# Kernel tuning notes

Hardware: AMD Instinct MI355X
Metric: run time of the kernel (lower is better)

The kernel has to match this reference:

```python
import jax, jax.numpy as jnp
import numpy as np

BETA = 1.0

def setup_inputs() -> dict:
    key = jax.random.key(0)
    k1, k2, k3 = jax.random.split(key, 3)
    B, T, G, D, V = 4, 2048, 8, 128, 1024
    inputs = jax.random.normal(k1, (B, T, G * D), dtype=jnp.float32)
    paddings = jax.random.randint(k2, (B, T), 0, 2, dtype=jnp.int32)
    codebook = jax.random.normal(k3, (V, G, D), dtype=jnp.float32)  # (V, G, D)
    return {"inputs": inputs, "paddings": paddings, "codebook": codebook}

def reference(inputs, paddings, codebook):
    B, T, _ = inputs.shape
    V, G, D = codebook.shape
    sg = jax.lax.stop_gradient
    x = inputs.reshape(B, T, G, D)
    x2 = jnp.sum(x * x, axis=-1)                      # (B,T,G)
    c2 = jnp.sum(codebook * codebook, axis=-1)        # (V,G)
    xc = jnp.einsum('btgd,vgd->btvg', x, codebook)    # (B,T,V,G) GEMM
    dist = x2[:, :, None, :] - 2.0 * xc + c2[None, None]
    ids = jnp.argmin(dist, axis=2)                    # (B,T,G) int
    # gather codebook[ids[b,t,g], g] -> (B,T,G,D)
    quantized = codebook[ids, jnp.arange(G)[None, None, :]]
    mask = (1 - paddings).astype(jnp.float32)[:, :, None, None]  # (B,T,1,1)
    msum = mask.sum()
    kmeans_loss = jnp.sum(((quantized - sg(x)) ** 2) * mask) / msum
    commitment_loss = jnp.sum(((x - sg(quantized)) ** 2) * mask) / msum
    total_loss = kmeans_loss + BETA * commitment_loss
    quantized_st = ((x + sg(quantized - x)) * mask).reshape(B, T, G * D)
    ids = jnp.where((paddings == 1)[:, :, None], -1, ids.astype(jnp.int32))
    return (ids, quantized_st, kmeans_loss, commitment_loss, total_loss)
```

## Files before the change

### kernel.cpp

```cpp
#include <hip/hip_runtime.h>
#include <math.h>

typedef _Float16 f16;
typedef f16 half8 __attribute__((ext_vector_type(8)));
typedef float f32x4 __attribute__((ext_vector_type(4)));

#define BT 8192
#define NG 8
#define ND 128
#define NV 1024
#define MARGIN  0.08f
#define MARGIN3 0.16f
#define BM 64
#define BN 64
#define NT 16
#define FULLBIT 0x40000000u

#define OUT_IDS 0
#define OUT_Q   65536
#define OUT_L   (65536 + 8388608)

#define OFF_C2A    0
#define OFF_C2B    8192
#define OFF_LOSSG  81920
#define OFF_CNT    147456
#define OFF_FLAGS  147464
#define OFF_CBH    213000
#define OFF_PART   (OFF_CBH + 524288)
#define OFF_CAND2  (OFF_PART + 64)
#define OFF_TOKMAP (OFF_CAND2 + 65536)

__device__ __forceinline__ void gll16(const f16* g, f16* l) {
    __builtin_amdgcn_global_load_lds(
        (const __attribute__((address_space(1))) unsigned int*)g,
        (__attribute__((address_space(3))) unsigned int*)l, 16, 0, 0);
}

__global__ __launch_bounds__(256) void prep_kernel(
    const float* __restrict__ cb, const int* __restrict__ pad,
    f16* __restrict__ cbh, float* __restrict__ c2a, float* __restrict__ c2b,
    int* __restrict__ ncnt, int* __restrict__ tokmap) {
    __shared__ float prod[16][16][9];
    __shared__ float rbuf[16][8];
    const int tid = threadIdx.x;
    const int rloc = tid >> 4, t = tid & 15;
    const int idx = blockIdx.x * 16 + rloc;
    const int v = idx >> 3, g = idx & 7;
    const int rl = v & 63;
    const float4* row4 = (const float4*)(cb + (size_t)idx * ND);

    if (tid < 16) {
        int tok = blockIdx.x * 16 + tid;
        if (!pad[tok]) {
            int p = atomicAdd(ncnt, 1);
            tokmap[p] = tok;
        }
    }

    float4 a = row4[t * 2], b = row4[t * 2 + 1];
    float vv[8] = {a.x, a.y, a.z, a.w, b.x, b.y, b.z, b.w};
    half8 h;
#pragma unroll
    for (int e = 0; e < 8; ++e) {
        prod[rloc][t][e] = __fmul_rn(vv[e], vv[e]);
        h[e] = (f16)vv[e];
    }
    int cn = v >> 6;
    size_t base = ((size_t)(g * 16 + cn)) * 8192 + rl * 128;
    *(half8*)(cbh + base + ((t ^ (rl & 7)) * 8)) = h;
    __syncthreads();

    if (t < 8) {
        float r = 0.f;
#pragma unroll
        for (int tt = 0; tt < 16; ++tt)
            r = __fadd_rn(r, prod[rloc][tt][t]);
        rbuf[rloc][t] = r;
    }
    __syncthreads();
    if (t == 0) {
        float s = __fadd_rn(
            __fadd_rn(__fadd_rn(rbuf[rloc][0], rbuf[rloc][1]),
                      __fadd_rn(rbuf[rloc][2], rbuf[rloc][3])),
            __fadd_rn(__fadd_rn(rbuf[rloc][4], rbuf[rloc][5]),
                      __fadd_rn(rbuf[rloc][6], rbuf[rloc][7])));
        c2a[idx] = s;
        c2b[g * NV + v] = s;
    }
}

__global__ __launch_bounds__(256) void padfill(
    const int* __restrict__ pad, float* __restrict__ out_ids,
    float* __restrict__ out_q, float* __restrict__ lossg) {
    const int tok = blockIdx.x;
    if (!pad[tok]) return;
    const int tid = threadIdx.x;
    ((float4*)(out_q + (size_t)tok * (NG * ND)))[tid] =
        make_float4(0.f, 0.f, 0.f, 0.f);
    if (tid < NG) {
        out_ids[tok * NG + tid] = -1.0f;
        lossg[tok * NG + tid] = 0.0f;
    }
}

__global__ __launch_bounds__(256, 4) void mfma_gemm(
    const float* __restrict__ x, const f16* __restrict__ cbh,
    const float* __restrict__ cb, const float* __restrict__ c2b,
    const int* __restrict__ ncnt, const int* __restrict__ tokmap,
    float* __restrict__ out_ids, float* __restrict__ out_q,
    float* __restrict__ lossg, int* __restrict__ cnt,
    int* __restrict__ flags, int* __restrict__ cand2) {
    __shared__ __align__(16) f16 Bh[2][BN * ND];
    __shared__ __align__(16) float c2s[NV];
    __shared__ int idsL[BM];
    __shared__ int tokL[BM];

    const int tid = threadIdx.x;
    const int b = blockIdx.x;
    const int g = b & 7;
    const int count = *ncnt;
    const int tile_base = (b >> 3) * BM;
    if (tile_base >= count) return;
    const int lane = tid & 63;
    const int w = tid >> 6;
    const int wr = w & 1, wc = w >> 1;
    const int l15 = lane & 15, l4 = lane >> 4;

    ((float4*)c2s)[tid] = ((const float4*)(c2b + (size_t)g * NV))[tid];
    {
        const f16* sh = cbh + ((size_t)(g * 16 + 0)) * 8192;
#pragma unroll
        for (int it = 0; it < 4; ++it)
            gll16(sh + it * 2048 + tid * 8, &Bh[0][it * 2048 + tid * 8]);
    }

    int tokA_[2];
#pragma unroll
    for (int ti = 0; ti < 2; ++ti) {
        int slot = tile_base + wr * 32 + ti * 16 + l15;
        tokA_[ti] = tokmap[(slot < count) ? slot : 0];
    }

    half8 ah[4][2];
#pragma unroll
    for (int kk = 0; kk < 4; ++kk)
#pragma unroll
        for (int ti = 0; ti < 2; ++ti) {
            const float* ap = x + ((size_t)tokA_[ti] * NG + g) * ND
                              + kk * 32 + l4 * 8;
            float4 p0 = *(const float4*)ap, p1 = *(const float4*)(ap + 4);
            float vv[8] = {p0.x, p0.y, p0.z, p0.w, p1.x, p1.y, p1.z, p1.w};
            half8 h;
#pragma unroll
            for (int j = 0; j < 8; ++j) h[j] = (f16)vv[j];
            ah[kk][ti] = h;
        }

    float d1s[2][4], d2s[2][4], d3s[2][4];
    int id1s[2][4], id2s[2][4];
#pragma unroll
    for (int ti = 0; ti < 2; ++ti)
#pragma unroll
        for (int r = 0; r < 4; ++r) {
            d1s[ti][r] = INFINITY;
            d2s[ti][r] = INFINITY;
            d3s[ti][r] = INFINITY;
            id1s[ti][r] = 0;
            id2s[ti][r] = 0;
        }

    int buf = 0;
#pragma unroll 1
    for (int t = 0; t < NT; ++t) {
        asm volatile("s_waitcnt vmcnt(0) lgkmcnt(0)" ::: "memory");
        __builtin_amdgcn_s_barrier();
        __builtin_amdgcn_sched_barrier(0);

        if (t + 1 < NT) {
            const f16* sh = cbh + ((size_t)(g * 16 + t + 1)) * 8192;
#pragma unroll
            for (int it = 0; it < 4; ++it)
                gll16(sh + it * 2048 + tid * 8,
                      &Bh[buf ^ 1][it * 2048 + tid * 8]);
        }

        f32x4 acc[2][2];
#pragma unroll
        for (int ti = 0; ti < 2; ++ti)
#pragma unroll
            for (int tj = 0; tj < 2; ++tj)
                acc[ti][tj] = (f32x4){0.f, 0.f, 0.f, 0.f};

#pragma unroll
        for (int kk = 0; kk < 4; ++kk) {
            half8 bh[2];
#pragma unroll
            for (int tj = 0; tj < 2; ++tj) {
                int rw = wc * 32 + tj * 16 + l15;
                bh[tj] = *(const half8*)(
                    &Bh[buf][rw * 128 + (((kk * 4 + l4) ^ (rw & 7)) << 3)]);
            }
#pragma unroll
            for (int ti = 0; ti < 2; ++ti)
#pragma unroll
                for (int tj = 0; tj < 2; ++tj)
                    acc[ti][tj] = __builtin_amdgcn_mfma_f32_16x16x32_f16(
                        ah[kk][ti], bh[tj], acc[ti][tj], 0, 0, 0);
        }

#pragma unroll
        for (int tj = 0; tj < 2; ++tj) {
            int code = t * BN + wc * 32 + tj * 16 + l15;
            float c2v = c2s[code];
#pragma unroll
            for (int ti = 0; ti < 2; ++ti)
#pragma unroll
                for (int r = 0; r < 4; ++r) {
                    float dv = fmaf(-2.0f, acc[ti][tj][r], c2v);
                    bool lt1 = dv < d1s[ti][r];
                    bool lt2 = dv < d2s[ti][r];
                    bool lt3 = dv < d3s[ti][r];
                    d3s[ti][r] = lt2 ? d2s[ti][r] : (lt3 ? dv : d3s[ti][r]);
                    d2s[ti][r] = lt1 ? d1s[ti][r] : (lt2 ? dv : d2s[ti][r]);
                    id2s[ti][r] = lt1 ? id1s[ti][r] : (lt2 ? code : id2s[ti][r]);
                    d1s[ti][r] = lt1 ? dv : d1s[ti][r];
                    id1s[ti][r] = lt1 ? code : id1s[ti][r];
                }
        }
        buf ^= 1;
    }

    __syncthreads();
    float4* red = (float4*)&Bh[0][0];
    float* redd3 = (float*)(red + 128);
#pragma unroll
    for (int ti = 0; ti < 2; ++ti)
#pragma unroll
        for (int r = 0; r < 4; ++r) {
            float d1 = d1s[ti][r], d2 = d2s[ti][r], d3 = d3s[ti][r];
            int i1 = id1s[ti][r], i2 = id2s[ti][r];
#pragma unroll
            for (int m = 1; m < 16; m <<= 1) {
                float od1 = __shfl_xor(d1, m);
                float od2 = __shfl_xor(d2, m);
                float od3 = __shfl_xor(d3, m);
                int oi1 = __shfl_xor(i1, m);
                int oi2 = __shfl_xor(i2, m);
                bool ow = od1 < d1;
                float w1 = ow ? od1 : d1, w2 = ow ? od2 : d2, w3 = ow ? od3 : d3;
                int wi1 = ow ? oi1 : i1, wi2 = ow ? oi2 : i2;
                float l1 = ow ? d1 : od1, l2 = ow ? d2 : od2;
                int li1 = ow ? i1 : oi1;
                d1 = w1; i1 = wi1;
                bool t2 = w2 < l1;
                d2 = t2 ? w2 : l1;
                i2 = t2 ? wi2 : li1;
                d3 = t2 ? fminf(w3, l1) : fminf(w2, l2);
            }
            if (l15 == 0) {
                int o = wc * BM + wr * 32 + ti * 16 + l4 * 4 + r;
                red[o] = make_float4(d1, __int_as_float(i1), d2,
                                     __int_as_float(i2));
                redd3[o] = d3;
            }
        }
    __syncthreads();

    if (tid < BM) {
        float4 A = red[tid], C = red[BM + tid];
        float a3 = redd3[tid], c3 = redd3[BM + tid];
        float a1 = A.x, a2 = A.z, c1 = C.x, c2q = C.z;
        int ai1 = __float_as_int(A.y), ai2 = __float_as_int(A.w);
        int ci1 = __float_as_int(C.y), ci2 = __float_as_int(C.w);
        bool cw = c1 < a1;
        float w1 = cw ? c1 : a1, w2 = cw ? c2q : a2, w3 = cw ? c3 : a3;
        int wi1 = cw ? ci1 : ai1, wi2 = cw ? ci2 : ai2;
        float l1 = cw ? a1 : c1, l2 = cw ? a2 : c2q;
        int li1 = cw ? ai1 : ci1;
        float d1 = w1;
        int i1 = wi1;
        bool t2 = w2 < l1;
        float d2 = t2 ? w2 : l1;
        int i2 = t2 ? wi2 : li1;
        float d3 = t2 ? fminf(w3, l1) : fminf(w2, l2);

        int slot = tile_base + tid;
        if (slot < count) {
            int tok = tokmap[slot];
            int idx = tok * NG + g;
            out_ids[idx] = (float)i1;
            idsL[tid] = i1;
            tokL[tid] = tok;
            if (d2 - d1 < MARGIN) {
                int pos = atomicAdd(cnt, 1);
                flags[pos] = idx;
                cand2[idx] = i2 | ((d3 - d1 < MARGIN3) ? (int)FULLBIT : 0);
            }
        } else {
            idsL[tid] = -1;
        }
    }
    __syncthreads();

#pragma unroll
    for (int it = 0; it < 8; ++it) {
        int i = it * 256 + tid;
        int tl = i >> 5, d4 = i & 31;
        int id = idsL[tl];
        if (id >= 0) {
            int tok = tokL[tl];
            size_t rowo = ((size_t)tok * NG + g) * ND;
            float4 q = ((const float4*)(cb + ((size_t)id * NG + g) * ND))[d4];
            float4 a = ((const float4*)(x + rowo))[d4];
            float e0 = q.x - a.x, e1 = q.y - a.y;
            float e2 = q.z - a.z, e3 = q.w - a.w;
            float s = e0 * e0 + e1 * e1 + e2 * e2 + e3 * e3;
            ((float4*)(out_q + rowo))[d4] = q;
#pragma unroll
            for (int m = 1; m < 32; m <<= 1) s += __shfl_xor(s, m);
            if (d4 == 0) lossg[tok * NG + g] = s;
        }
    }
}

__global__ __launch_bounds__(256) void recheck(
    const float* __restrict__ x, const float* __restrict__ cb,
    const float* __restrict__ c2w, const int* __restrict__ cnt,
    const int* __restrict__ flags, const int* __restrict__ cand2,
    float* __restrict__ out_ids, float* __restrict__ out_q,
    float* __restrict__ lossg) {
    __shared__ __align__(16) float xs[ND];
    __shared__ float2 redw[4];
    __shared__ int bidS;
    const int tid = threadIdx.x;
    const int lane = tid & 63;
    const int w = tid >> 6;
    const int n_f = cnt[0];

    for (int f = blockIdx.x * 4 + w; f < n_f; f += gridDim.x * 4) {
        int idx = flags[f];
        unsigned cc = (unsigned)cand2[idx];
        if (cc & FULLBIT) continue;
        int g = idx & 7;
        int id1 = (int)out_ids[idx];
        int id2 = (int)(cc & ~FULLBIT);
        float2 xv = ((const float2*)(x + (size_t)idx * ND))[lane];
        float2 av = ((const float2*)(cb + ((size_t)id1 * NG + g) * ND))[lane];
        float2 bv = ((const float2*)(cb + ((size_t)id2 * NG + g) * ND))[lane];
        float eA0 = xv.x - av.x, eA1 = xv.y - av.y;
        float eB0 = xv.x - bv.x, eB1 = xv.y - bv.y;
        float sA = eA0 * eA0 + eA1 * eA1;
        float sB = eB0 * eB0 + eB1 * eB1;
#pragma unroll
        for (int m = 1; m < 64; m <<= 1) {
            sA += __shfl_xor(sA, m);
            sB += __shfl_xor(sB, m);
        }
        int win;
        float sw;
        if (sA < sB) { win = id1; sw = sA; }
        else if (sB < sA) { win = id2; sw = sB; }
        else { win = (id1 < id2) ? id1 : id2; sw = sA; }
        if (win != id1) {
            if (lane == 0) {
                out_ids[idx] = (float)win;
                lossg[idx] = sw;
            }
            if (lane < 32) {
                float4 q = ((const float4*)(cb + ((size_t)win * NG + g) * ND))[lane];
                ((float4*)(out_q + (size_t)idx * ND))[lane] = q;
            }
        }
    }
    __syncthreads();

    for (int f = blockIdx.x; f < n_f; f += gridDim.x) {
        int idx = flags[f];
        if (!(((unsigned)cand2[idx]) & FULLBIT)) continue;
        int g = idx & 7;
        __syncthreads();
        if (tid < 32)
            ((float4*)xs)[tid] = ((const float4*)(x + (size_t)idx * ND))[tid];
        __syncthreads();

        float rr[8];
#pragma unroll
        for (int j = 0; j < 8; ++j) rr[j] = 0.0f;
#pragma unroll
        for (int i = 0; i < 32; ++i) {
            float4 v = ((const float4*)xs)[i];
            int j0 = (i * 4) & 7;
            rr[j0 + 0] = __fadd_rn(rr[j0 + 0], __fmul_rn(v.x, v.x));
            rr[j0 + 1] = __fadd_rn(rr[j0 + 1], __fmul_rn(v.y, v.y));
            rr[j0 + 2] = __fadd_rn(rr[j0 + 2], __fmul_rn(v.z, v.z));
            rr[j0 + 3] = __fadd_rn(rr[j0 + 3], __fmul_rn(v.w, v.w));
        }
        float x2v = __fadd_rn(
            __fadd_rn(__fadd_rn(rr[0], rr[1]), __fadd_rn(rr[2], rr[3])),
            __fadd_rn(__fadd_rn(rr[4], rr[5]), __fadd_rn(rr[6], rr[7])));

        float best = INFINITY;
        int bid = 0x7FFFFFFF;
        float s0 = 0.f, s1 = 0.f, s2 = 0.f, s3 = 0.f;
#pragma unroll
        for (int i = 0; i < 32; ++i) {
            float4 a = ((const float4*)xs)[i];
            float4 q0 = ((const float4*)(cb + ((size_t)(tid) * NG + g) * ND))[i];
            float4 q1 = ((const float4*)(cb + ((size_t)(tid + 256) * NG + g) * ND))[i];
            float4 q2 = ((const float4*)(cb + ((size_t)(tid + 512) * NG + g) * ND))[i];
            float4 q3 = ((const float4*)(cb + ((size_t)(tid + 768) * NG + g) * ND))[i];
            s0 = fmaf(a.x, q0.x, s0); s0 = fmaf(a.y, q0.y, s0);
            s0 = fmaf(a.z, q0.z, s0); s0 = fmaf(a.w, q0.w, s0);
            s1 = fmaf(a.x, q1.x, s1); s1 = fmaf(a.y, q1.y, s1);
            s1 = fmaf(a.z, q1.z, s1); s1 = fmaf(a.w, q1.w, s1);
            s2 = fmaf(a.x, q2.x, s2); s2 = fmaf(a.y, q2.y, s2);
            s2 = fmaf(a.z, q2.z, s2); s2 = fmaf(a.w, q2.w, s2);
            s3 = fmaf(a.x, q3.x, s3); s3 = fmaf(a.y, q3.y, s3);
            s3 = fmaf(a.z, q3.z, s3); s3 = fmaf(a.w, q3.w, s3);
        }
        float dd[4] = {s0, s1, s2, s3};
#pragma unroll
        for (int jj = 0; jj < 4; ++jj) {
            int c = tid + 256 * jj;
            float d = __fadd_rn(__fsub_rn(x2v, __fmul_rn(2.0f, dd[jj])),
                                c2w[(size_t)c * NG + g]);
            if (d < best || (d == best && c < bid)) { best = d; bid = c; }
        }
#pragma unroll
        for (int m = 1; m < 64; m <<= 1) {
            float od = __shfl_xor(best, m);
            int ob = __shfl_xor(bid, m);
            if (od < best || (od == best && ob < bid)) { best = od; bid = ob; }
        }
        if (lane == 0) redw[w] = make_float2(best, __int_as_float(bid));
        __syncthreads();
        if (tid == 0) {
            float b2 = redw[0].x;
            int i2 = __float_as_int(redw[0].y);
#pragma unroll
            for (int ww = 1; ww < 4; ++ww) {
                float ob = redw[ww].x;
                int oi = __float_as_int(redw[ww].y);
                if (ob < b2 || (ob == b2 && oi < i2)) { b2 = ob; i2 = oi; }
            }
            out_ids[idx] = (float)i2;
            bidS = i2;
        }
        __syncthreads();
        if (tid < 32) {
            float4 q = ((const float4*)(cb + ((size_t)bidS * NG + g) * ND))[tid];
            ((float4*)(out_q + (size_t)idx * ND))[tid] = q;
            float4 a = ((const float4*)xs)[tid];
            float e0 = q.x - a.x, e1 = q.y - a.y;
            float e2 = q.z - a.z, e3 = q.w - a.w;
            float s = e0 * e0 + e1 * e1 + e2 * e2 + e3 * e3;
#pragma unroll
            for (int m = 1; m < 32; m <<= 1) s += __shfl_xor(s, m);
            if (tid == 0) lossg[idx] = s;
        }
    }
}

__global__ __launch_bounds__(256) void loss_part(
    const float* __restrict__ lossg, float* __restrict__ part) {
    __shared__ float sr[256];
    const int tid = threadIdx.x;
    float4 v = ((const float4*)lossg)[blockIdx.x * 256 + tid];
    sr[tid] = ((v.x + v.y) + (v.z + v.w));
    __syncthreads();
    for (int st = 128; st > 0; st >>= 1) {
        if (tid < st) sr[tid] += sr[tid + st];
        __syncthreads();
    }
    if (tid == 0) part[blockIdx.x] = sr[0];
}

__global__ __launch_bounds__(256) void final_kernel(
    const int* __restrict__ pad, const float* __restrict__ part,
    float* __restrict__ out_l) {
    __shared__ int mr[256];
    const int tid = threadIdx.x;
    int m = 0;
#pragma unroll
    for (int i = 0; i < 32; ++i) m += 1 - pad[tid * 32 + i];
    mr[tid] = m;
    __syncthreads();
    for (int st = 128; st > 0; st >>= 1) {
        if (tid < st) mr[tid] += mr[tid + st];
        __syncthreads();
    }
    if (tid == 0) {
        float s = 0.f;
#pragma unroll
        for (int i = 0; i < 64; ++i) s += part[i];
        float k = s / (float)mr[0];
        out_l[0] = k;
        out_l[1] = k;
        out_l[2] = k + k;
    }
}

extern "C" void kernel_launch(void* const* d_in, const int* in_sizes, int n_in,
                              void* d_out, int out_size, void* d_ws, size_t ws_size,
                              hipStream_t stream) {
    const float* x = (const float*)d_in[0];
    const int* pad = (const int*)d_in[1];
    const float* cb = (const float*)d_in[2];
    float* out = (float*)d_out;
    float* ws = (float*)d_ws;

    float* ws_c2a = ws + OFF_C2A;
    float* ws_c2b = ws + OFF_C2B;
    float* ws_lossg = ws + OFF_LOSSG;
    int* ws_cnt = (int*)(ws + OFF_CNT);
    int* ws_flags = (int*)(ws + OFF_FLAGS);
    f16* cbh = (f16*)(ws + OFF_CBH);
    float* ws_part = ws + OFF_PART;
    int* ws_cand2 = (int*)(ws + OFF_CAND2);
    int* ws_tokmap = (int*)(ws + OFF_TOKMAP);

    hipMemsetAsync(ws_cnt, 0, 8, stream);
    prep_kernel<<<NV * NG / 16, 256, 0, stream>>>(cb, pad, cbh, ws_c2a,
                                                  ws_c2b, ws_cnt + 1,
                                                  ws_tokmap);
    padfill<<<BT, 256, 0, stream>>>(pad, out + OUT_IDS, out + OUT_Q, ws_lossg);
    mfma_gemm<<<(BT / BM) * NG, 256, 0, stream>>>(x, cbh, cb, ws_c2b,
                                                  ws_cnt + 1, ws_tokmap,
                                                  out + OUT_IDS, out + OUT_Q,
                                                  ws_lossg, ws_cnt, ws_flags,
                                                  ws_cand2);
    recheck<<<512, 256, 0, stream>>>(x, cb, ws_c2a, ws_cnt, ws_flags,
                                     ws_cand2, out + OUT_IDS, out + OUT_Q,
                                     ws_lossg);
    loss_part<<<64, 256, 0, stream>>>(ws_lossg, ws_part);
    final_kernel<<<1, 256, 0, stream>>>(pad, ws_part, out + OUT_L);
}
```

Before: 85.08 us.

## Halve GEMM row tile and split codes across four waves; replace memset with kernel

The row tile of the distance GEMM shrinks from 64 to 32 tokens, giving twice as many blocks. Each of the four waves now owns 16 codes of the 64-code column tile instead of a 2x2 wave grid, and the cross-wave top-3 merge is generalised to four partials. The hipMemsetAsync that clears the counters is replaced by a tiny zero kernel. More blocks should raise occupancy on the many-CU GPU, but each block now streams the same codebook tiles for half as many rows, doubling codebook traffic per token.

```diff
diff --git a/kernel.cpp b/kernel.cpp
--- a/kernel.cpp
+++ b/kernel.cpp
@@ -11,7 +11,7 @@
 #define NV 1024
 #define MARGIN  0.08f
 #define MARGIN3 0.16f
-#define BM 64
+#define BM 32
 #define BN 64
 #define NT 16
 #define FULLBIT 0x40000000u
@@ -34,6 +34,10 @@
     __builtin_amdgcn_global_load_lds(
         (const __attribute__((address_space(1))) unsigned int*)g,
         (__attribute__((address_space(3))) unsigned int*)l, 16, 0, 0);
+}
+
+__global__ void zero_kernel(int* __restrict__ cnt) {
+    if (threadIdx.x < 2) cnt[threadIdx.x] = 0;
 }
 
 __global__ __launch_bounds__(256) void prep_kernel(
@@ -123,8 +127,8 @@
     if (tile_base >= count) return;
     const int lane = tid & 63;
     const int w = tid >> 6;
-    const int wr = w & 1, wc = w >> 1;
     const int l15 = lane & 15, l4 = lane >> 4;
+    const int rw = w * 16 + l15;
 
     ((float4*)c2s)[tid] = ((const float4*)(c2b + (size_t)g * NV))[tid];
     {
@@ -137,7 +141,7 @@
     int tokA_[2];
 #pragma unroll
     for (int ti = 0; ti < 2; ++ti) {
-        int slot = tile_base + wr * 32 + ti * 16 + l15;
+        int slot = tile_base + ti * 16 + l15;
         tokA_[ti] = tokmap[(slot < count) ? slot : 0];
     }
 
@@ -184,39 +188,28 @@
                       &Bh[buf ^ 1][it * 2048 + tid * 8]);
         }
 
-        f32x4 acc[2][2];
-#pragma unroll
-        for (int ti = 0; ti < 2; ++ti)
-#pragma unroll
-            for (int tj = 0; tj < 2; ++tj)
-                acc[ti][tj] = (f32x4){0.f, 0.f, 0.f, 0.f};
+        f32x4 acc[2];
+#pragma unroll
+        for (int ti = 0; ti < 2; ++ti) acc[ti] = (f32x4){0.f, 0.f, 0.f, 0.f};
 
 #pragma unroll
         for (int kk = 0; kk < 4; ++kk) {
-            half8 bh[2];
-#pragma unroll
-            for (int tj = 0; tj < 2; ++tj) {
-                int rw = wc * 32 + tj * 16 + l15;
-                bh[tj] = *(const half8*)(
-                    &Bh[buf][rw * 128 + (((kk * 4 + l4) ^ (rw & 7)) << 3)]);
-            }
+            half8 bh = *(const half8*)(
+                &Bh[buf][rw * 128 + (((kk * 4 + l4) ^ (rw & 7)) << 3)]);
 #pragma unroll
             for (int ti = 0; ti < 2; ++ti)
-#pragma unroll
-                for (int tj = 0; tj < 2; ++tj)
-                    acc[ti][tj] = __builtin_amdgcn_mfma_f32_16x16x32_f16(
-                        ah[kk][ti], bh[tj], acc[ti][tj], 0, 0, 0);
-        }
-
-#pragma unroll
-        for (int tj = 0; tj < 2; ++tj) {
-            int code = t * BN + wc * 32 + tj * 16 + l15;
+                acc[ti] = __builtin_amdgcn_mfma_f32_16x16x32_f16(
+                    ah[kk][ti], bh, acc[ti], 0, 0, 0);
+        }
+
+        {
+            int code = t * BN + rw;
             float c2v = c2s[code];
 #pragma unroll
             for (int ti = 0; ti < 2; ++ti)
 #pragma unroll
                 for (int r = 0; r < 4; ++r) {
-                    float dv = fmaf(-2.0f, acc[ti][tj][r], c2v);
+                    float dv = fmaf(-2.0f, acc[ti][r], c2v);
                     bool lt1 = dv < d1s[ti][r];
                     bool lt2 = dv < d2s[ti][r];
                     bool lt3 = dv < d3s[ti][r];
@@ -258,7 +251,7 @@
                 d3 = t2 ? fminf(w3, l1) : fminf(w2, l2);
             }
             if (l15 == 0) {
-                int o = wc * BM + wr * 32 + ti * 16 + l4 * 4 + r;
+                int o = w * BM + ti * 16 + l4 * 4 + r;
                 red[o] = make_float4(d1, __int_as_float(i1), d2,
                                      __int_as_float(i2));
                 redd3[o] = d3;
@@ -267,22 +260,25 @@
     __syncthreads();
 
     if (tid < BM) {
-        float4 A = red[tid], C = red[BM + tid];
-        float a3 = redd3[tid], c3 = redd3[BM + tid];
-        float a1 = A.x, a2 = A.z, c1 = C.x, c2q = C.z;
-        int ai1 = __float_as_int(A.y), ai2 = __float_as_int(A.w);
-        int ci1 = __float_as_int(C.y), ci2 = __float_as_int(C.w);
-        bool cw = c1 < a1;
-        float w1 = cw ? c1 : a1, w2 = cw ? c2q : a2, w3 = cw ? c3 : a3;
-        int wi1 = cw ? ci1 : ai1, wi2 = cw ? ci2 : ai2;
-        float l1 = cw ? a1 : c1, l2 = cw ? a2 : c2q;
-        int li1 = cw ? ai1 : ci1;
-        float d1 = w1;
-        int i1 = wi1;
-        bool t2 = w2 < l1;
-        float d2 = t2 ? w2 : l1;
-        int i2 = t2 ? wi2 : li1;
-        float d3 = t2 ? fminf(w3, l1) : fminf(w2, l2);
+        float4 A = red[tid];
+        float d1 = A.x, d2 = A.z, d3 = redd3[tid];
+        int i1 = __float_as_int(A.y), i2 = __float_as_int(A.w);
+#pragma unroll
+        for (int ww = 1; ww < 4; ++ww) {
+            float4 C = red[ww * BM + tid];
+            float e1 = C.x, e2 = C.z, e3 = redd3[ww * BM + tid];
+            int j1 = __float_as_int(C.y), j2 = __float_as_int(C.w);
+            bool ow = e1 < d1;
+            float w1 = ow ? e1 : d1, w2 = ow ? e2 : d2, w3 = ow ? e3 : d3;
+            int wi1 = ow ? j1 : i1, wi2 = ow ? j2 : i2;
+            float l1 = ow ? d1 : e1, l2 = ow ? d2 : e2;
+            int li1 = ow ? i1 : j1;
+            d1 = w1; i1 = wi1;
+            bool t2 = w2 < l1;
+            d2 = t2 ? w2 : l1;
+            i2 = t2 ? wi2 : li1;
+            d3 = t2 ? fminf(w3, l1) : fminf(w2, l2);
+        }
 
         int slot = tile_base + tid;
         if (slot < count) {
@@ -303,7 +299,7 @@
     __syncthreads();
 
 #pragma unroll
-    for (int it = 0; it < 8; ++it) {
+    for (int it = 0; it < 4; ++it) {
         int i = it * 256 + tid;
         int tl = i >> 5, d4 = i & 31;
         int id = idsL[tl];
@@ -519,7 +515,7 @@
     int* ws_cand2 = (int*)(ws + OFF_CAND2);
     int* ws_tokmap = (int*)(ws + OFF_TOKMAP);
 
-    hipMemsetAsync(ws_cnt, 0, 8, stream);
+    zero_kernel<<<1, 64, 0, stream>>>(ws_cnt);
     prep_kernel<<<NV * NG / 16, 256, 0, stream>>>(cb, pad, cbh, ws_c2a,
                                                   ws_c2b, ws_cnt + 1,
                                                   ws_tokmap);
```

Measured after the change: 88.13 us. +3.6%, slower.
